# Optimization experiments

Measured on AMD Instinct MI355X. Metric: run time of the kernel, lower is better.

## Reference

```python
import jax, jax.numpy as jnp
import numpy as np

N_NODES = 50000
N_EDGES = 800000
N_SCALARS = 32
NUM_REP = 8
L_MAX = 4
DIST_DIM = 64
X_DIM = N_SCALARS + NUM_REP * L_MAX * 2  # 96
HIDDEN = 128
MSG_IN = 2 * X_DIM + DIST_DIM  # 256


def setup_inputs() -> dict:
    key = jax.random.key(0)
    ks = jax.random.split(key, 9)
    return {
        "x_scalar": jax.random.normal(ks[0], (N_NODES, N_SCALARS), jnp.float32),
        "x_rot": jax.random.normal(ks[1], (N_NODES, NUM_REP, L_MAX * 2), jnp.float32),
        "edge_index": jax.random.randint(ks[2], (2, N_EDGES), 0, N_NODES),
        "distance_embedding": jax.random.normal(ks[3], (N_EDGES, DIST_DIM), jnp.float32),
        "rot": jax.random.normal(ks[4], (N_EDGES, L_MAX, 2, 2), jnp.float32),
        "W1": jax.random.normal(ks[5], (MSG_IN, HIDDEN), jnp.float32) * (1.0 / np.sqrt(MSG_IN)),
        "b1": jnp.zeros((HIDDEN,), jnp.float32),
        "W2": jax.random.normal(ks[6], (HIDDEN, X_DIM), jnp.float32) * (1.0 / np.sqrt(HIDDEN)),
        "b2": jnp.zeros((X_DIM,), jnp.float32),
    }


def _rotate(x_edges, R):
    # x_edges: [E, num_rep, L_max*2] -> rotate each (L_max, 2) pair by R: [E, L_max, 2, 2]
    E = x_edges.shape[0]
    xr = x_edges.reshape(E, NUM_REP, L_MAX, 2)
    return jnp.einsum('njkm,nkml->njkl', xr, R).reshape(E, NUM_REP * L_MAX * 2)


def reference(x_scalar, x_rot, edge_index, distance_embedding, rot, W1, b1, W2, b2):
    row, col = edge_index[0], edge_index[1]
    E = row.shape[0]
    N = x_scalar.shape[0]
    rot_inv = jnp.swapaxes(rot, 2, 3)  # transpose(rot, 2, 3)

    # gather + per-edge rotation into edge frame, concat with scalars
    x_src = jnp.concatenate([x_scalar[row], _rotate(x_rot[row], rot_inv)], axis=1)  # [E, x_dim]
    x_dst = jnp.concatenate([x_scalar[col], _rotate(x_rot[col], rot_inv)], axis=1)  # [E, x_dim]

    # message MLP (stand-in for TransformerMessage): out dim = x_dim
    h = jax.nn.silu(jnp.concatenate([x_dst, x_src, distance_embedding], axis=1) @ W1 + b1)
    x_out = h @ W2 + b2  # [E, x_dim]

    mess_scalar = x_out[:, :N_SCALARS]
    mr = x_out[:, N_SCALARS:].reshape(E, NUM_REP, L_MAX, 2)
    mess_rot = jnp.einsum('njkm,nkml->njkl', mr, rot).reshape(E, NUM_REP, L_MAX * 2)

    out_rot = jax.ops.segment_sum(mess_rot, col, num_segments=N)      # [N, num_rep, L_max*2]
    out_scalar = jax.ops.segment_sum(mess_scalar, col, num_segments=N)  # [N, n_scalars]
    return (out_scalar, out_rot)
```

## Files before the change

kernel.cpp:

```cpp
#include <hip/hip_runtime.h>

#define N_NODES  50000
#define N_EDGES  800000
#define NSC      32
#define XD       96
#define HID      128
#define MSG      256
#define LDH      136
#define LDXO     100
#define NBLK     196
#define NTILES   50000
#define TPW      25

typedef __bf16 bf16x8 __attribute__((ext_vector_type(8)));
typedef float  f32x4  __attribute__((ext_vector_type(4)));
typedef unsigned short u16x8 __attribute__((ext_vector_type(8)));

__device__ __forceinline__ unsigned short f2bf(float f) {
    union { float f; unsigned int u; } v; v.f = f;
    unsigned int u = v.u;
    return (unsigned short)((u + 0x7FFFu + ((u >> 16) & 1u)) >> 16);
}
__device__ __forceinline__ float bflo(unsigned int u) {
    union { unsigned int u; float f; } v; v.u = u << 16; return v.f;
}
__device__ __forceinline__ float bfhi(unsigned int u) {
    union { unsigned int u; float f; } v; v.u = u & 0xffff0000u; return v.f;
}

#define WAVE_SYNC() do { \
    asm volatile("s_waitcnt lgkmcnt(0)" ::: "memory"); \
    __builtin_amdgcn_sched_barrier(0); \
} while (0)

__global__ void prep_weights(const float* __restrict__ W1, const float* __restrict__ W2,
                             unsigned short* __restrict__ W1R, unsigned short* __restrict__ W2R) {
    int o = blockIdx.x * 256 + threadIdx.x;
    if (o < 32 * 128 * 8) {
        int j = o & 7, ch = o >> 3;
        int n = ch & 127, kt = ch >> 7;
        W1R[o] = f2bf(W1[(kt * 8 + j) * 128 + n]);
    }
    if (o < 16 * 96 * 8) {
        int j = o & 7, ch = o >> 3;
        int n = ch % 96, kt = ch / 96;
        W2R[o] = f2bf(W2[(kt * 8 + j) * 96 + n]);
    }
}

__global__ void rank0_kernel(const int* __restrict__ eidx, int* __restrict__ cnt,
                             int* __restrict__ pos0) {
    int e = blockIdx.x * 256 + threadIdx.x;
    if (e < N_EDGES) pos0[e] = atomicAdd(&cnt[eidx[N_EDGES + e]], 1);
}

__global__ void scan_block(const int* __restrict__ cnt, int* __restrict__ start,
                           int* __restrict__ bsum) {
    __shared__ int tmp[256];
    const int t = threadIdx.x, i = blockIdx.x * 256 + t;
    int v = (i < N_NODES) ? cnt[i] : 0;
    tmp[t] = v; __syncthreads();
    #pragma unroll
    for (int off = 1; off < 256; off <<= 1) {
        int add = (t >= off) ? tmp[t - off] : 0;
        __syncthreads();
        tmp[t] += add;
        __syncthreads();
    }
    if (i < N_NODES) start[i] = tmp[t] - v;
    if (t == 255) bsum[blockIdx.x] = tmp[255];
}

__global__ void scan_top(const int* __restrict__ bsum, int* __restrict__ boff,
                         int* __restrict__ start) {
    __shared__ int tmp[256];
    const int t = threadIdx.x;
    int v = (t < NBLK) ? bsum[t] : 0;
    tmp[t] = v; __syncthreads();
    #pragma unroll
    for (int off = 1; off < 256; off <<= 1) {
        int add = (t >= off) ? tmp[t - off] : 0;
        __syncthreads();
        tmp[t] += add;
        __syncthreads();
    }
    if (t < NBLK) boff[t] = tmp[t] - v;
    if (t == 255) start[N_NODES] = tmp[255];
}

__global__ void scan_fix(int* __restrict__ start, const int* __restrict__ boff) {
    const int t = threadIdx.x, i = blockIdx.x * 256 + t;
    if (i < N_NODES) start[i] += boff[blockIdx.x];
}

__global__ void scatter_kernel(const int* __restrict__ eidx, const int* __restrict__ start,
                               const int* __restrict__ pos0, int4* __restrict__ srt) {
    int e = blockIdx.x * 256 + threadIdx.x;
    if (e < N_EDGES) {
        int r = eidx[e];
        int c = eidx[N_EDGES + e];
        int slot = start[c] + pos0[e];
        srt[slot] = make_int4(e, r, c, 0);
    }
}

__global__ __launch_bounds__(512, 2)
void eq_main_sorted(const float* __restrict__ x_scalar, const float* __restrict__ x_rot,
                    const float* __restrict__ dist, const float* __restrict__ rot,
                    const unsigned short* __restrict__ W1R, const float* __restrict__ b1,
                    const unsigned short* __restrict__ W2R, const float* __restrict__ b2,
                    const int4* __restrict__ srt, unsigned int* __restrict__ msg)
{
    __shared__ unsigned char SH[155648];
    unsigned char* W1L = SH;
    unsigned char* W2L = SH + 65536;

    const int tid  = threadIdx.x;
    const int wave = tid >> 6, lane = tid & 63;
    unsigned char* tile = SH + 90112 + wave * 8192;

    {
        const uint4* g1 = (const uint4*)W1R;  uint4* l1 = (uint4*)W1L;
        #pragma unroll
        for (int i = 0; i < 8; ++i) l1[i * 512 + tid] = g1[i * 512 + tid];
        const uint4* g2 = (const uint4*)W2R;  uint4* l2 = (uint4*)W2L;
        #pragma unroll
        for (int i = 0; i < 3; ++i) l2[i * 512 + tid] = g2[i * 512 + tid];
    }
    __syncthreads();

    const int eL = lane >> 2, p = lane & 3;
    const int lrow = lane & 15, quad = lane >> 4;

    const int g  = blockIdx.x * 8 + wave;
    int t0 = g * TPW, t1 = t0 + TPW;
    if (t1 > NTILES) t1 = NTILES;

    for (int t = t0; t < t1; ++t) {
        const int slot = t * 16 + eL;
        const int4 erc = srt[slot];
        const int e = erc.x, r = erc.y, c = erc.z;

        float rb[16];
        {
            const float4* rp = (const float4*)(rot + (size_t)e * 16);
            #pragma unroll
            for (int i = 0; i < 4; ++i) ((float4*)rb)[i] = rp[i];
        }

        {
            const float *baseA, *baseB; bool rotA, rotB;
            if (p == 0)      { baseA = x_scalar + (size_t)c * NSC;     rotA = false;
                               baseB = x_rot    + (size_t)c * 64;      rotB = true;  }
            else if (p == 1) { baseA = x_rot    + (size_t)c * 64 + 32; rotA = true;
                               baseB = x_scalar + (size_t)r * NSC;     rotB = false; }
            else if (p == 2) { baseA = x_rot    + (size_t)r * 64;      rotA = true;
                               baseB = x_rot    + (size_t)r * 64 + 32; rotB = true;  }
            else             { baseA = dist     + (size_t)e * 64;      rotA = false;
                               baseB = dist     + (size_t)e * 64 + 32; rotB = false; }

            #pragma unroll
            for (int i = 0; i < 8; ++i) {
                const float* src  = (i < 4) ? (baseA + i * 8) : (baseB + (i - 4) * 8);
                const bool  isrot = (i < 4) ? rotA : rotB;
                float4 v0 = ((const float4*)src)[0], v1 = ((const float4*)src)[1];
                float x[8] = { v0.x, v0.y, v0.z, v0.w, v1.x, v1.y, v1.z, v1.w };
                u16x8 tt;
                #pragma unroll
                for (int k = 0; k < 4; ++k) {
                    float a0 = x[2 * k], a1 = x[2 * k + 1];
                    float r0 = a0 * rb[4 * k]     + a1 * rb[4 * k + 1];
                    float r1 = a0 * rb[4 * k + 2] + a1 * rb[4 * k + 3];
                    tt[2 * k]     = f2bf(isrot ? r0 : a0);
                    tt[2 * k + 1] = f2bf(isrot ? r1 : a1);
                }
                const int ci = p * 8 + i;
                *(u16x8*)&tile[(eL << 9) + ((ci * 16) ^ ((eL & 7) << 4))] = tt;
            }
        }
        WAVE_SYNC();

        f32x4 acc[8];
        #pragma unroll
        for (int j = 0; j < 8; ++j) acc[j] = (f32x4){0.f, 0.f, 0.f, 0.f};
        #pragma unroll
        for (int kk = 0; kk < 8; ++kk) {
            bf16x8 a = *(const bf16x8*)&tile[(lrow << 9) +
                                             ((kk * 64 + quad * 16) ^ ((lrow & 7) << 4))];
            const unsigned char* wb = W1L + ((kk * 4 + quad) * 128) * 16;
            #pragma unroll
            for (int j = 0; j < 8; ++j) {
                bf16x8 b = *(const bf16x8*)(wb + (j * 16 + lrow) * 16);
                acc[j] = __builtin_amdgcn_mfma_f32_16x16x32_bf16(a, b, acc[j], 0, 0, 0);
            }
        }
        WAVE_SYNC();

        unsigned short* H16 = (unsigned short*)tile;
        #pragma unroll
        for (int j = 0; j < 8; ++j) {
            const int n = j * 16 + lrow;
            const float bv = b1[n];
            #pragma unroll
            for (int rr = 0; rr < 4; ++rr) {
                const int m = quad * 4 + rr;
                float v = acc[j][rr] + bv;
                float hv = v / (1.0f + __expf(-v));
                H16[m * LDH + n] = f2bf(hv);
            }
        }
        WAVE_SYNC();

        f32x4 acc2[6];
        #pragma unroll
        for (int j = 0; j < 6; ++j) acc2[j] = (f32x4){0.f, 0.f, 0.f, 0.f};
        #pragma unroll
        for (int kk = 0; kk < 4; ++kk) {
            bf16x8 a = *(const bf16x8*)&H16[lrow * LDH + kk * 32 + quad * 8];
            const unsigned char* wb = W2L + ((kk * 4 + quad) * 96) * 16;
            #pragma unroll
            for (int j = 0; j < 6; ++j) {
                bf16x8 b = *(const bf16x8*)(wb + (j * 16 + lrow) * 16);
                acc2[j] = __builtin_amdgcn_mfma_f32_16x16x32_bf16(a, b, acc2[j], 0, 0, 0);
            }
        }
        WAVE_SYNC();

        float* XOf = (float*)tile;
        #pragma unroll
        for (int j = 0; j < 6; ++j) {
            const int n = j * 16 + lrow;
            const float bv = b2[n];
            #pragma unroll
            for (int rr = 0; rr < 4; ++rr) {
                const int m = quad * 4 + rr;
                XOf[m * LDXO + n] = acc2[j][rr] + bv;
            }
        }
        WAVE_SYNC();

        {
            const float* xo = XOf + eL * LDXO;
            unsigned int buf[12];
            #pragma unroll
            for (int q = 0; q < 12; ++q) {
                const int i = p * 24 + 2 * q;
                float v0 = xo[i], v1 = xo[i + 1];
                if (i >= NSC) {
                    const int k = ((i - NSC) >> 1) & 3;
                    float a0 = v0, a1 = v1;
                    v0 = a0 * rb[4 * k + 0] + a1 * rb[4 * k + 2];
                    v1 = a0 * rb[4 * k + 1] + a1 * rb[4 * k + 3];
                }
                buf[q] = (unsigned int)f2bf(v0) | ((unsigned int)f2bf(v1) << 16);
            }
            unsigned int* mrow = msg + (size_t)slot * 48 + p * 12;
            *(uint4*)(mrow + 0) = *(uint4*)(buf + 0);
            *(uint4*)(mrow + 4) = *(uint4*)(buf + 4);
            *(uint4*)(mrow + 8) = *(uint4*)(buf + 8);
        }
        WAVE_SYNC();
    }
}

__global__ __launch_bounds__(256, 2)
void eq_main_atomic(const float* __restrict__ x_scalar, const float* __restrict__ x_rot,
                    const int* __restrict__ eidx, const float* __restrict__ dist,
                    const float* __restrict__ rot,
                    const unsigned short* __restrict__ W1R, const float* __restrict__ b1,
                    const unsigned short* __restrict__ W2R, const float* __restrict__ b2,
                    float* __restrict__ out_scalar, float* __restrict__ out_rot)
{
    __shared__ union { unsigned char B[64 * 512]; float XO[64 * LDXO]; } uA;
    __shared__ unsigned short H[64 * LDH];
    __shared__ int colidx[64];

    const int tid = threadIdx.x;
    const int e0  = blockIdx.x * 64;

    {
        const int eL = tid >> 2, p = tid & 3;
        const int e  = e0 + eL;
        if (e < N_EDGES) {
            const int r = eidx[e];
            const int c = eidx[N_EDGES + e];
            if (p == 0) colidx[eL] = c;
            float rb[16];
            {
                const float4* rp = (const float4*)(rot + (size_t)e * 16);
                #pragma unroll
                for (int i = 0; i < 4; ++i) ((float4*)rb)[i] = rp[i];
            }
            const float *baseA, *baseB; bool rotA, rotB;
            if (p == 0)      { baseA = x_scalar + (size_t)c * NSC;     rotA = false;
                               baseB = x_rot    + (size_t)c * 64;      rotB = true;  }
            else if (p == 1) { baseA = x_rot    + (size_t)c * 64 + 32; rotA = true;
                               baseB = x_scalar + (size_t)r * NSC;     rotB = false; }
            else if (p == 2) { baseA = x_rot    + (size_t)r * 64;      rotA = true;
                               baseB = x_rot    + (size_t)r * 64 + 32; rotB = true;  }
            else             { baseA = dist     + (size_t)e * 64;      rotA = false;
                               baseB = dist     + (size_t)e * 64 + 32; rotB = false; }
            #pragma unroll
            for (int i = 0; i < 8; ++i) {
                const float* src  = (i < 4) ? (baseA + i * 8) : (baseB + (i - 4) * 8);
                const bool  isrot = (i < 4) ? rotA : rotB;
                float4 v0 = ((const float4*)src)[0], v1 = ((const float4*)src)[1];
                float x[8] = { v0.x, v0.y, v0.z, v0.w, v1.x, v1.y, v1.z, v1.w };
                u16x8 tt;
                #pragma unroll
                for (int k = 0; k < 4; ++k) {
                    float a0 = x[2 * k], a1 = x[2 * k + 1];
                    float r0 = a0 * rb[4 * k]     + a1 * rb[4 * k + 1];
                    float r1 = a0 * rb[4 * k + 2] + a1 * rb[4 * k + 3];
                    tt[2 * k]     = f2bf(isrot ? r0 : a0);
                    tt[2 * k + 1] = f2bf(isrot ? r1 : a1);
                }
                const int ci = p * 8 + i;
                *(u16x8*)&uA.B[(eL << 9) + ((ci * 16) ^ ((eL & 7) << 4))] = tt;
            }
        }
    }
    __syncthreads();

    const int lane = tid & 63, wave = tid >> 6;
    const int lrow = lane & 15, quad = lane >> 4;
    const int m0 = wave * 16;

    {
        f32x4 acc[8];
        #pragma unroll
        for (int j = 0; j < 8; ++j) acc[j] = (f32x4){0.f, 0.f, 0.f, 0.f};
        #pragma unroll
        for (int kk = 0; kk < 8; ++kk) {
            bf16x8 a = *(const bf16x8*)&uA.B[((m0 + lrow) << 9) +
                                             ((kk * 64 + quad * 16) ^ ((lrow & 7) << 4))];
            const unsigned short* wb = W1R + (size_t)(kk * 4 + quad) * 1024;
            #pragma unroll
            for (int j = 0; j < 8; ++j) {
                bf16x8 b = *(const bf16x8*)(wb + (j * 16 + lrow) * 8);
                acc[j] = __builtin_amdgcn_mfma_f32_16x16x32_bf16(a, b, acc[j], 0, 0, 0);
            }
        }
        __syncthreads();
        #pragma unroll
        for (int j = 0; j < 8; ++j) {
            const int n = j * 16 + lrow;
            const float bv = b1[n];
            #pragma unroll
            for (int rr = 0; rr < 4; ++rr) {
                const int m = m0 + quad * 4 + rr;
                float v = acc[j][rr] + bv;
                float hv = v / (1.0f + __expf(-v));
                H[m * LDH + n] = f2bf(hv);
            }
        }
    }
    __syncthreads();

    {
        f32x4 acc2[6];
        #pragma unroll
        for (int j = 0; j < 6; ++j) acc2[j] = (f32x4){0.f, 0.f, 0.f, 0.f};
        #pragma unroll
        for (int kk = 0; kk < 4; ++kk) {
            bf16x8 a = *(const bf16x8*)&H[(m0 + lrow) * LDH + kk * 32 + quad * 8];
            const unsigned short* wb = W2R + (size_t)(kk * 4 + quad) * 768;
            #pragma unroll
            for (int j = 0; j < 6; ++j) {
                bf16x8 b = *(const bf16x8*)(wb + (j * 16 + lrow) * 8);
                acc2[j] = __builtin_amdgcn_mfma_f32_16x16x32_bf16(a, b, acc2[j], 0, 0, 0);
            }
        }
        __syncthreads();
        #pragma unroll
        for (int j = 0; j < 6; ++j) {
            const int n = j * 16 + lrow;
            const float bv = b2[n];
            #pragma unroll
            for (int rr = 0; rr < 4; ++rr) {
                const int m = m0 + quad * 4 + rr;
                float v = acc2[j][rr] + bv;
                if (j < 2) {
                    if (e0 + m < N_EDGES)
                        atomicAdd(&out_scalar[(size_t)colidx[m] * NSC + n], v);
                } else {
                    uA.XO[m * LDXO + (n - NSC)] = v;
                }
            }
        }
    }
    __syncthreads();

    {
        const int eL = tid >> 2, p = tid & 3;
        const int e  = e0 + eL;
        if (e < N_EDGES) {
            float rb[16];
            {
                const float4* rp = (const float4*)(rot + (size_t)e * 16);
                #pragma unroll
                for (int i = 0; i < 4; ++i) ((float4*)rb)[i] = rp[i];
            }
            const int c = colidx[eL];
            const float* xo = &uA.XO[eL * LDXO];
            float* outp = out_rot + (size_t)c * 64;
            #pragma unroll
            for (int jj = 0; jj < 2; ++jj) {
                const int j = 2 * p + jj;
                #pragma unroll
                for (int k = 0; k < 4; ++k) {
                    float a0 = xo[j * 8 + k * 2], a1 = xo[j * 8 + k * 2 + 1];
                    atomicAdd(&outp[j * 8 + k * 2 + 0], a0 * rb[4 * k + 0] + a1 * rb[4 * k + 2]);
                    atomicAdd(&outp[j * 8 + k * 2 + 1], a0 * rb[4 * k + 1] + a1 * rb[4 * k + 3]);
                }
            }
        }
    }
}

__global__ __launch_bounds__(256)
void gather_kernel(const unsigned int* __restrict__ msg, const int* __restrict__ start,
                   float* __restrict__ out_scalar, float* __restrict__ out_rot) {
    const int wave = threadIdx.x >> 6, lane = threadIdx.x & 63;
    const int n = blockIdx.x * 4 + wave;
    if (n >= N_NODES) return;
    const int s = start[n], e = start[n + 1];
    if (lane < 48) {
        float a0 = 0.f, a1 = 0.f;
        const unsigned int* p = msg + (size_t)s * 48 + lane;
        int i = s;
        for (; i + 1 < e; i += 2) {
            unsigned int u0 = p[0], u1 = p[48];
            p += 96;
            a0 += bflo(u0) + bflo(u1);
            a1 += bfhi(u0) + bfhi(u1);
        }
        if (i < e) { unsigned int u = p[0]; a0 += bflo(u); a1 += bfhi(u); }
        const int col = lane * 2;
        float2 r = make_float2(a0, a1);
        if (col < NSC) *(float2*)(out_scalar + (size_t)n * NSC + col) = r;
        else           *(float2*)(out_rot   + (size_t)n * 64 + (col - NSC)) = r;
    }
}

extern "C" void kernel_launch(void* const* d_in, const int* in_sizes, int n_in,
                              void* d_out, int out_size, void* d_ws, size_t ws_size,
                              hipStream_t stream) {
    const float* x_scalar = (const float*)d_in[0];
    const float* x_rot    = (const float*)d_in[1];
    const int*   eidx     = (const int*)d_in[2];
    const float* dist     = (const float*)d_in[3];
    const float* rot      = (const float*)d_in[4];
    const float* W1       = (const float*)d_in[5];
    const float* b1       = (const float*)d_in[6];
    const float* W2       = (const float*)d_in[7];
    const float* b2       = (const float*)d_in[8];
    float* out        = (float*)d_out;
    float* out_rot    = out + (size_t)N_NODES * NSC;

    uintptr_t base = (uintptr_t)d_ws;
    auto alloc = [&](size_t bytes) {
        uintptr_t p = base; base += (bytes + 255) & ~(size_t)255; return p;
    };
    unsigned short* W1R  = (unsigned short*)alloc(256 * 128 * 2);
    unsigned short* W2R  = (unsigned short*)alloc(128 * 96 * 2);
    int*            cnt  = (int*)alloc(N_NODES * 4);
    int*            start= (int*)alloc((N_NODES + 1) * 4);
    int*            bsum = (int*)alloc(NBLK * 4);
    int*            boff = (int*)alloc(NBLK * 4);
    int*            pos0 = (int*)alloc((size_t)N_EDGES * 4);
    int4*           srt  = (int4*)alloc((size_t)N_EDGES * 16);
    unsigned int*   msg  = (unsigned int*)alloc((size_t)N_EDGES * 48 * 4);
    const size_t needed = base - (uintptr_t)d_ws;

    prep_weights<<<128, 256, 0, stream>>>(W1, W2, W1R, W2R);

    if (ws_size >= needed) {
        hipMemsetAsync(cnt, 0, N_NODES * 4, stream);
        rank0_kernel<<<N_EDGES / 256, 256, 0, stream>>>(eidx, cnt, pos0);
        scan_block<<<NBLK, 256, 0, stream>>>(cnt, start, bsum);
        scan_top<<<1, 256, 0, stream>>>(bsum, boff, start);
        scan_fix<<<NBLK, 256, 0, stream>>>(start, boff);
        scatter_kernel<<<N_EDGES / 256, 256, 0, stream>>>(eidx, start, pos0, srt);
        eq_main_sorted<<<256, 512, 0, stream>>>(
            x_scalar, x_rot, dist, rot, W1R, b1, W2R, b2, srt, msg);
        gather_kernel<<<(N_NODES + 3) / 4, 256, 0, stream>>>(msg, start, out, out_rot);
    } else {
        hipMemsetAsync(d_out, 0, (size_t)out_size * sizeof(float), stream);
        eq_main_atomic<<<N_EDGES / 64, 256, 0, stream>>>(
            x_scalar, x_rot, eidx, dist, rot, W1R, b1, W2R, b2,
            out, out_rot);
    }
}
```

Measured before the change: 611.5 us.

## Fuse segmented reduction into main kernel and software-prefetch next tile gathers

Removes the bf16 message buffer and the separate gather kernel. Each wave now keeps a running per-column sum over the destination-sorted edges and atomically adds it to the output whenever the destination changes, with the output zeroed by a memset first. The gathers for the next tile (features, distances, rotations, sorted index) are issued before the current tile's MLP, to hide gather latency behind the MFMA work. This costs more registers for the prefetched tile, which may lower occupancy, and it adds atomics where a node's edges span wave boundaries. Sums are also no longer rounded through bf16 messages.

Result: no change. 623.5 us (+2.0%).

```diff
diff --git a/kernel.cpp b/kernel.cpp
--- a/kernel.cpp
+++ b/kernel.cpp
@@ -5,7 +5,6 @@
 #define NSC      32
 #define XD       96
 #define HID      128
-#define MSG      256
 #define LDH      136
 #define LDXO     100
 #define NBLK     196
@@ -20,12 +19,6 @@
     union { float f; unsigned int u; } v; v.f = f;
     unsigned int u = v.u;
     return (unsigned short)((u + 0x7FFFu + ((u >> 16) & 1u)) >> 16);
-}
-__device__ __forceinline__ float bflo(unsigned int u) {
-    union { unsigned int u; float f; } v; v.u = u << 16; return v.f;
-}
-__device__ __forceinline__ float bfhi(unsigned int u) {
-    union { unsigned int u; float f; } v; v.u = u & 0xffff0000u; return v.f;
 }
 
 #define WAVE_SYNC() do { \
@@ -109,7 +102,8 @@
                     const float* __restrict__ dist, const float* __restrict__ rot,
                     const unsigned short* __restrict__ W1R, const float* __restrict__ b1,
                     const unsigned short* __restrict__ W2R, const float* __restrict__ b2,
-                    const int4* __restrict__ srt, unsigned int* __restrict__ msg)
+                    const int4* __restrict__ srt,
+                    float* __restrict__ out_scalar, float* __restrict__ out_rot)
 {
     __shared__ unsigned char SH[155648];
     unsigned char* W1L = SH;
@@ -118,6 +112,10 @@
     const int tid  = threadIdx.x;
     const int wave = tid >> 6, lane = tid & 63;
     unsigned char* tile = SH + 90112 + wave * 8192;
+    float*          XOf = (float*)tile;
+    float*          rbL = (float*)(tile + 6400);
+    int*            cLs = (int*)(tile + 7424);
+    unsigned short* H16 = (unsigned short*)tile;
 
     {
         const uint4* g1 = (const uint4*)W1R;  uint4* l1 = (uint4*)W1L;
@@ -135,35 +133,62 @@
     const int g  = blockIdx.x * 8 + wave;
     int t0 = g * TPW, t1 = t0 + TPW;
     if (t1 > NTILES) t1 = NTILES;
+    if (t0 >= t1) return;
+
+    float4 cA[16], cRb4[4];
+    int4 ercC, ercN;
+
+    auto addr_sel = [&](const int4& er, const float*& baseA, const float*& baseB) {
+        const int e = er.x, r = er.y, c = er.z;
+        if (p == 0)      { baseA = x_scalar + (size_t)c * NSC;
+                           baseB = x_rot    + (size_t)c * 64;      }
+        else if (p == 1) { baseA = x_rot    + (size_t)c * 64 + 32;
+                           baseB = x_scalar + (size_t)r * NSC;     }
+        else if (p == 2) { baseA = x_rot    + (size_t)r * 64;
+                           baseB = x_rot    + (size_t)r * 64 + 32; }
+        else             { baseA = dist     + (size_t)e * 64;
+                           baseB = dist     + (size_t)e * 64 + 32; }
+        (void)0;
+        return e;
+    };
+
+    #define ISSUE_PREFETCH(ER, PA, PR) do { \
+        const float *bA_, *bB_; \
+        const int e_ = addr_sel(ER, bA_, bB_); \
+        const float4* rp_ = (const float4*)(rot + (size_t)e_ * 16); \
+        _Pragma("unroll") \
+        for (int i_ = 0; i_ < 4; ++i_) (PR)[i_] = rp_[i_]; \
+        _Pragma("unroll") \
+        for (int i_ = 0; i_ < 4; ++i_) { \
+            (PA)[2*i_]     = ((const float4*)(bA_ + i_*8))[0]; \
+            (PA)[2*i_ + 1] = ((const float4*)(bA_ + i_*8))[1]; \
+            (PA)[8 + 2*i_] = ((const float4*)(bB_ + i_*8))[0]; \
+            (PA)[9 + 2*i_] = ((const float4*)(bB_ + i_*8))[1]; \
+        } \
+    } while (0)
+
+    ercC = srt[t0 * 16 + eL];
+    ISSUE_PREFETCH(ercC, cA, cRb4);
+    {
+        int tn = (t0 + 1 < t1) ? t0 + 1 : t0;
+        ercN = srt[tn * 16 + eL];
+    }
+
+    const int c0 = 2 * lane;
+    float acc0 = 0.f, acc1 = 0.f;
+    int prevc = -1;
 
     for (int t = t0; t < t1; ++t) {
-        const int slot = t * 16 + eL;
-        const int4 erc = srt[slot];
-        const int e = erc.x, r = erc.y, c = erc.z;
-
-        float rb[16];
         {
-            const float4* rp = (const float4*)(rot + (size_t)e * 16);
-            #pragma unroll
-            for (int i = 0; i < 4; ++i) ((float4*)rb)[i] = rp[i];
-        }
-
-        {
-            const float *baseA, *baseB; bool rotA, rotB;
-            if (p == 0)      { baseA = x_scalar + (size_t)c * NSC;     rotA = false;
-                               baseB = x_rot    + (size_t)c * 64;      rotB = true;  }
-            else if (p == 1) { baseA = x_rot    + (size_t)c * 64 + 32; rotA = true;
-                               baseB = x_scalar + (size_t)r * NSC;     rotB = false; }
-            else if (p == 2) { baseA = x_rot    + (size_t)r * 64;      rotA = true;
-                               baseB = x_rot    + (size_t)r * 64 + 32; rotB = true;  }
-            else             { baseA = dist     + (size_t)e * 64;      rotA = false;
-                               baseB = dist     + (size_t)e * 64 + 32; rotB = false; }
-
+            float rb[16];
+            #pragma unroll
+            for (int i = 0; i < 4; ++i) ((float4*)rb)[i] = cRb4[i];
+            const bool rotA = (p == 1) || (p == 2);
+            const bool rotB = (p == 0) || (p == 2);
             #pragma unroll
             for (int i = 0; i < 8; ++i) {
-                const float* src  = (i < 4) ? (baseA + i * 8) : (baseB + (i - 4) * 8);
-                const bool  isrot = (i < 4) ? rotA : rotB;
-                float4 v0 = ((const float4*)src)[0], v1 = ((const float4*)src)[1];
+                const bool isrot = (i < 4) ? rotA : rotB;
+                float4 v0 = cA[2 * i], v1 = cA[2 * i + 1];
                 float x[8] = { v0.x, v0.y, v0.z, v0.w, v1.x, v1.y, v1.z, v1.w };
                 u16x8 tt;
                 #pragma unroll
@@ -178,6 +203,15 @@
                 *(u16x8*)&tile[(eL << 9) + ((ci * 16) ^ ((eL & 7) << 4))] = tt;
             }
         }
+
+        float4 nA[16], nRb4[4];
+        ISSUE_PREFETCH(ercN, nA, nRb4);
+        int4 ercN2;
+        {
+            int tn2 = (t + 2 < t1) ? t + 2 : t;
+            ercN2 = srt[tn2 * 16 + eL];
+        }
+
         WAVE_SYNC();
 
         f32x4 acc[8];
@@ -196,7 +230,6 @@
         }
         WAVE_SYNC();
 
-        unsigned short* H16 = (unsigned short*)tile;
         #pragma unroll
         for (int j = 0; j < 8; ++j) {
             const int n = j * 16 + lrow;
@@ -209,6 +242,12 @@
                 H16[m * LDH + n] = f2bf(hv);
             }
         }
+        {
+            float4 w = (p == 0) ? cRb4[0] : (p == 1) ? cRb4[1]
+                     : (p == 2) ? cRb4[2] : cRb4[3];
+            *(float4*)&rbL[eL * 16 + 4 * p] = w;
+            if (p == 0) cLs[eL] = ercC.z;
+        }
         WAVE_SYNC();
 
         f32x4 acc2[6];
@@ -226,7 +265,6 @@
         }
         WAVE_SYNC();
 
-        float* XOf = (float*)tile;
         #pragma unroll
         for (int j = 0; j < 6; ++j) {
             const int n = j * 16 + lrow;
@@ -239,28 +277,49 @@
         }
         WAVE_SYNC();
 
-        {
-            const float* xo = XOf + eL * LDXO;
-            unsigned int buf[12];
-            #pragma unroll
-            for (int q = 0; q < 12; ++q) {
-                const int i = p * 24 + 2 * q;
-                float v0 = xo[i], v1 = xo[i + 1];
-                if (i >= NSC) {
-                    const int k = ((i - NSC) >> 1) & 3;
+        if (lane < 48) {
+            #pragma unroll
+            for (int rI = 0; rI < 16; ++rI) {
+                float2 v = *(const float2*)&XOf[rI * LDXO + c0];
+                float v0 = v.x, v1 = v.y;
+                if (c0 >= NSC) {
+                    const int k = ((c0 - NSC) >> 1) & 3;
+                    const float4 R = *(const float4*)&rbL[rI * 16 + 4 * k];
                     float a0 = v0, a1 = v1;
-                    v0 = a0 * rb[4 * k + 0] + a1 * rb[4 * k + 2];
-                    v1 = a0 * rb[4 * k + 1] + a1 * rb[4 * k + 3];
+                    v0 = a0 * R.x + a1 * R.z;
+                    v1 = a0 * R.y + a1 * R.w;
                 }
-                buf[q] = (unsigned int)f2bf(v0) | ((unsigned int)f2bf(v1) << 16);
-            }
-            unsigned int* mrow = msg + (size_t)slot * 48 + p * 12;
-            *(uint4*)(mrow + 0) = *(uint4*)(buf + 0);
-            *(uint4*)(mrow + 4) = *(uint4*)(buf + 4);
-            *(uint4*)(mrow + 8) = *(uint4*)(buf + 8);
+                int cr = cLs[rI];
+                if (cr != prevc) {
+                    if (prevc >= 0) {
+                        float* bp = (c0 < NSC)
+                            ? (out_scalar + (size_t)prevc * NSC + c0)
+                            : (out_rot    + (size_t)prevc * 64 + (c0 - NSC));
+                        atomicAdd(bp,     acc0);
+                        atomicAdd(bp + 1, acc1);
+                    }
+                    acc0 = 0.f; acc1 = 0.f; prevc = cr;
+                }
+                acc0 += v0; acc1 += v1;
+            }
         }
         WAVE_SYNC();
-    }
+
+        #pragma unroll
+        for (int i = 0; i < 16; ++i) cA[i] = nA[i];
+        #pragma unroll
+        for (int i = 0; i < 4; ++i) cRb4[i] = nRb4[i];
+        ercC = ercN; ercN = ercN2;
+    }
+
+    if (lane < 48 && prevc >= 0) {
+        float* bp = (c0 < NSC)
+            ? (out_scalar + (size_t)prevc * NSC + c0)
+            : (out_rot    + (size_t)prevc * 64 + (c0 - NSC));
+        atomicAdd(bp,     acc0);
+        atomicAdd(bp + 1, acc1);
+    }
+    #undef ISSUE_PREFETCH
 }
 
 __global__ __launch_bounds__(256, 2)
@@ -418,31 +477,6 @@
     }
 }
 
-__global__ __launch_bounds__(256)
-void gather_kernel(const unsigned int* __restrict__ msg, const int* __restrict__ start,
-                   float* __restrict__ out_scalar, float* __restrict__ out_rot) {
-    const int wave = threadIdx.x >> 6, lane = threadIdx.x & 63;
-    const int n = blockIdx.x * 4 + wave;
-    if (n >= N_NODES) return;
-    const int s = start[n], e = start[n + 1];
-    if (lane < 48) {
-        float a0 = 0.f, a1 = 0.f;
-        const unsigned int* p = msg + (size_t)s * 48 + lane;
-        int i = s;
-        for (; i + 1 < e; i += 2) {
-            unsigned int u0 = p[0], u1 = p[48];
-            p += 96;
-            a0 += bflo(u0) + bflo(u1);
-            a1 += bfhi(u0) + bfhi(u1);
-        }
-        if (i < e) { unsigned int u = p[0]; a0 += bflo(u); a1 += bfhi(u); }
-        const int col = lane * 2;
-        float2 r = make_float2(a0, a1);
-        if (col < NSC) *(float2*)(out_scalar + (size_t)n * NSC + col) = r;
-        else           *(float2*)(out_rot   + (size_t)n * 64 + (col - NSC)) = r;
-    }
-}
-
 extern "C" void kernel_launch(void* const* d_in, const int* in_sizes, int n_in,
                               void* d_out, int out_size, void* d_ws, size_t ws_size,
                               hipStream_t stream) {
@@ -470,10 +504,10 @@
     int*            boff = (int*)alloc(NBLK * 4);
     int*            pos0 = (int*)alloc((size_t)N_EDGES * 4);
     int4*           srt  = (int4*)alloc((size_t)N_EDGES * 16);
-    unsigned int*   msg  = (unsigned int*)alloc((size_t)N_EDGES * 48 * 4);
     const size_t needed = base - (uintptr_t)d_ws;
 
     prep_weights<<<128, 256, 0, stream>>>(W1, W2, W1R, W2R);
+    hipMemsetAsync(d_out, 0, (size_t)out_size * sizeof(float), stream);
 
     if (ws_size >= needed) {
         hipMemsetAsync(cnt, 0, N_NODES * 4, stream);
@@ -483,10 +517,8 @@
         scan_fix<<<NBLK, 256, 0, stream>>>(start, boff);
         scatter_kernel<<<N_EDGES / 256, 256, 0, stream>>>(eidx, start, pos0, srt);
         eq_main_sorted<<<256, 512, 0, stream>>>(
-            x_scalar, x_rot, dist, rot, W1R, b1, W2R, b2, srt, msg);
-        gather_kernel<<<(N_NODES + 3) / 4, 256, 0, stream>>>(msg, start, out, out_rot);
+            x_scalar, x_rot, dist, rot, W1R, b1, W2R, b2, srt, out, out_rot);
     } else {
-        hipMemsetAsync(d_out, 0, (size_t)out_size * sizeof(float), stream);
         eq_main_atomic<<<N_EDGES / 64, 256, 0, stream>>>(
             x_scalar, x_rot, eidx, dist, rot, W1R, b1, W2R, b2,
             out, out_rot);
```
